# Performance work log

Hardware: AMD Instinct MI355X
Metric: run time of the kernel (lower is better)

## Reference

```python
import jax, jax.numpy as jnp
import numpy as np

B, T, D = 64, 64, 64
E, HA, HB, OUT = 128, 128, 128, 1
SHORT = 2


def _rn(k, shape, scale=0.05):
    return jax.random.normal(k, shape, dtype=jnp.float32) * scale


def setup_inputs() -> dict:
    key = jax.random.key(0)
    ks = jax.random.split(key, 18)
    return {
        "x": jax.random.normal(ks[0], (B, T, D), dtype=jnp.float32),
        "W_emb": _rn(ks[1], (E, D)), "b_emb": _rn(ks[2], (E,)),
        "Wi_a": _rn(ks[3], (3 * HA, E)), "Wh_a": _rn(ks[4], (3 * HA, HA)),
        "bi_a": _rn(ks[5], (3 * HA,)), "bh_a": _rn(ks[6], (3 * HA,)),
        "Wi_b": _rn(ks[7], (3 * HB, E)), "Wh_b": _rn(ks[8], (3 * HB, HB)),
        "bi_b": _rn(ks[9], (3 * HB,)), "bh_b": _rn(ks[10], (3 * HB,)),
        "Wa": _rn(ks[11], (1, HA)), "ba": _rn(ks[12], (1,)),
        "Wb": _rn(ks[13], (E, HB)), "bb": _rn(ks[14], (E,)),
        "Wo": _rn(ks[15], (OUT, E)), "bo": _rn(ks[16], (OUT,)),
        "short": SHORT,
    }


def _gru_cell(x, h, Wi, Wh, bi, bh):
    # PyTorch GRU cell: gates ordered (r, z, n)
    gi = x @ Wi.T + bi
    gh = h @ Wh.T + bh
    ir, iz, in_ = jnp.split(gi, 3, axis=-1)
    hr, hz, hn = jnp.split(gh, 3, axis=-1)
    r = jax.nn.sigmoid(ir + hr)
    z = jax.nn.sigmoid(iz + hz)
    n = jnp.tanh(in_ + r * hn)
    return (1.0 - z) * n + z * h


def _forward(x, W_emb, b_emb, Wi_a, Wh_a, bi_a, bh_a, Wi_b, Wh_b, bi_b, bh_b,
             Wa, ba, Wb, bb, Wo, bo, short):
    Bn, Tn = x.shape[0], x.shape[1]
    temp = jnp.transpose(x, (1, 0, 2))            # [T, B, D]
    emb = temp @ W_emb.T + b_emb                  # [T, B, E]
    P = Tn - 1                                    # prefix p handles att_timesteps t = p+1
    S = Tn - 1                                    # max reversed-prefix length
    p_idx = jnp.arange(P)
    h0a = jnp.zeros((P, Bn, Wh_a.shape[1]), x.dtype)
    h0b = jnp.zeros((P, Bn, Wh_b.shape[1]), x.dtype)

    # All prefixes at once: for prefix p, reversed input at step s is emb[p - s].
    def step(carry, s):
        ha, hb = carry
        j = jnp.clip(p_idx - s, 0, Tn - 1)        # [P]
        e_in = emb[j]                             # [P, B, E]
        x_in = temp[j]                            # [P, B, D]
        na = _gru_cell(e_in, ha, Wi_a, Wh_a, bi_a, bh_a)
        nb = _gru_cell(e_in, hb, Wi_b, Wh_b, bi_b, bh_b)
        valid = (p_idx >= s)[:, None, None]
        ha = jnp.where(valid, na, ha)
        hb = jnp.where(valid, nb, hb)
        return (ha, hb), (ha, hb, e_in, x_in)

    _, (Ha, Hb, Eg, Xg) = jax.lax.scan(step, (h0a, h0b), jnp.arange(S))
    Ha = 0.5 * Ha                                 # reverse_h_a * 0.5, [S, P, B, HA]
    Hb = 0.5 * Hb                                 # reverse_h_b * 0.5, [S, P, B, HB]

    mask = p_idx[None, :] >= jnp.arange(S)[:, None]   # [S, P] valid scan steps
    preA = jnp.einsum('spbh,h->spb', Ha, Wa[0]) + ba[0]
    preA = jnp.where(mask[:, :, None], preA, -jnp.inf)
    alpha = jax.nn.softmax(preA, axis=0)              # softmax over prefix positions
    beta = jnp.tanh(jnp.einsum('spbh,eh->spbe', Hb, Wb) + bb)  # [S, P, B, E]

    # context: c[p] = sum_s alpha * beta * emb[p-s]  (softmax is order-invariant)
    c = jnp.einsum('spb,spbe->pbe', alpha, beta * Eg)          # [P, B, E]
    pred = c @ Wo.T + bo                                        # [P, B, 1]

    # interpretability weights: e = (beta * w_out) @ W_emb, f = alpha*e*x, g = mean over prefix
    e_chain = jnp.einsum('spbe,ed->spbd', beta * Wo[0], W_emb)  # [S, P, B, D]
    f = alpha[..., None] * e_chain * Xg
    g = jnp.sum(f, axis=0) / (p_idx[:, None, None] + 1.0)       # mean over t = p+1 steps

    pred = jnp.transpose(pred[short + 1:], (1, 0, 2))           # [B, T-2-short, 1]
    weight = jnp.transpose(g[short + 1:], (1, 0, 2))            # [B, T-2-short, D]
    return pred, weight


def reference(x, W_emb, b_emb, Wi_a, Wh_a, bi_a, bh_a, Wi_b, Wh_b, bi_b, bh_b,
              Wa, ba, Wb, bb, Wo, bo, short):
    return _forward(x, W_emb, b_emb, Wi_a, Wh_a, bi_a, bh_a, Wi_b, Wh_b, bi_b,
                    bh_b, Wa, ba, Wb, bb, Wo, bo, short)
```

## Files before the change

### kernel.cpp

```cpp
#include <hip/hip_runtime.h>
#include <hip/hip_bf16.h>
#include <math.h>

#define B_ 64
#define T_ 64
#define D_ 64
#define PMIN 3
#define NPOUT 60
#define NCHUNK 8

typedef __hip_bfloat16 bf16;
typedef __attribute__((ext_vector_type(4))) short s16x4;
typedef __attribute__((ext_vector_type(8))) short s16x8;
typedef __attribute__((ext_vector_type(4))) float f32x4;

#define OFF_EMB   0
#define OFF_WIC   524288
#define OFF_XT    622592
#define OFF_GIPK  884736
#define OFF_WPK   2457600
#define OFF_BPPK  2506752
#define OFF_WMPK  2514944
#define OFF_WALPK 2519040
#define OFF_FLAG  2520064

__device__ __forceinline__ float bf2f(unsigned short u) {
    union { float f; unsigned u32; } x; x.u32 = ((unsigned)u) << 16; return x.f;
}
__device__ __forceinline__ unsigned short f2bf(float f) {
    union { float f; unsigned u; } x; x.f = f;
    unsigned r = x.u + 0x7FFFu + ((x.u >> 16) & 1u);
    return (unsigned short)(r >> 16);
}
__device__ __forceinline__ float LDF(const void* p, int i, int flag) {
    return flag ? ((const float*)p)[i] : bf2f(((const unsigned short*)p)[i]);
}
__device__ __forceinline__ float sigmoidf_(float v) { return 1.f / (1.f + __expf(-v)); }
__device__ __forceinline__ float tanhf_(float v) {
    float e = __expf(-2.f * fabsf(v));
    float t = (1.f - e) / (1.f + e);
    return copysignf(t, v);
}
__device__ __forceinline__ int kpi(int s) {
    return (s & ~31) | ((s & 1) << 4) | ((s & 31) >> 1);
}
__device__ __forceinline__ s16x8 ldA(const short* p) {
    s16x4 lo = *(const s16x4*)p;
    s16x4 hi = *(const s16x4*)(p + 4);
    return __builtin_shufflevector(lo, hi, 0, 1, 2, 3, 4, 5, 6, 7);
}

__global__ void detect_dtype(const unsigned short* xr, int* flag)
{
    int tid = threadIdx.x;
    int bad = 0;
    for (int i = tid; i < 4096; i += 256) {
        int ex = (xr[i] >> 7) & 0xFF;
        if (ex >= 140) bad++;
    }
    __shared__ int s[256];
    s[tid] = bad;
    __syncthreads();
    for (int st = 128; st > 0; st >>= 1) {
        if (tid < st) s[tid] += s[tid + st];
        __syncthreads();
    }
    if (tid == 0) *flag = (s[0] > 4) ? 1 : 0;
}

__global__ void prep_all(const void* p_x, const void* p_wemb, const void* p_bemb,
                         const void* p_wia, const void* p_wha,
                         const void* p_wib, const void* p_whb,
                         const void* p_wa, const void* p_wb, const void* p_wo,
                         float* ws, const int* flagp)
{
    const int flag = *flagp;
    int id = blockIdx.x * 256 + threadIdx.x;
    if (id < 98304) {
        int e = id / 768, g = id % 768;
        float v = (g < 384) ? LDF(p_wia, g * 128 + e, flag)
                            : LDF(p_wib, (g - 384) * 128 + e, flag);
        ws[OFF_WIC + id] = v;
    } else if (id < 622592) {
        int id2 = id - 98304;
        int e = id2 & 127;
        int tb = id2 >> 7;
        int b = tb & 63, t = tb >> 6;
        float acc = LDF(p_bemb, e, flag);
        if (flag) {
            const float* xp = (const float*)p_x + (b * T_ + t) * D_;
            const float* wp = (const float*)p_wemb + e * D_;
            #pragma unroll
            for (int d = 0; d < 64; d += 4) {
                f32x4 xv = *(const f32x4*)(xp + d);
                f32x4 wv = *(const f32x4*)(wp + d);
                acc += xv[0]*wv[0] + xv[1]*wv[1] + xv[2]*wv[2] + xv[3]*wv[3];
            }
        } else {
            const unsigned short* xp = (const unsigned short*)p_x + (b * T_ + t) * D_;
            const unsigned short* wp = (const unsigned short*)p_wemb + e * D_;
            for (int d = 0; d < 64; d++) acc += bf2f(xp[d]) * bf2f(wp[d]);
        }
        ws[OFF_EMB + id2] = acc;
    } else if (id < 884736) {
        int id5 = id - 622592;
        int b = id5 & 63, d = (id5 >> 6) & 63, t = id5 >> 12;
        ws[OFF_XT + id5] = LDF(p_x, (b * 64 + t) * 64 + d, flag);
    } else if (id < 983040) {
        unsigned short* wpk = (unsigned short*)(ws + OFF_WPK);
        int id3 = id - 884736;
        int w = id3 / 12288, r1 = id3 % 12288;
        int nt = r1 / 2048, r2 = r1 % 2048;
        int kt = r2 / 512, r3 = r2 % 512;
        int lane = r3 >> 3, j = r3 & 7;
        int cell = w >> 2, wv = w & 3;
        int gate = nt >> 1, tt = nt & 1;
        int g = gate * 128 + wv * 32 + tt * 16 + (lane & 15);
        int k = kpi(kt * 32 + (lane >> 4) * 8 + j);
        wpk[id3] = f2bf(LDF(cell ? p_whb : p_wha, g * 128 + k, flag));
    } else if (id < 999424) {
        unsigned short* bpk = (unsigned short*)(ws + OFF_BPPK);
        int id4 = id - 983040;
        int w = id4 / 2048, r = id4 % 2048;
        int kt = r / 512, lane = (r % 512) >> 3, j = r & 7;
        int e = w * 16 + (lane & 15);
        int k = kpi(kt * 32 + (lane >> 4) * 8 + j);
        bpk[id4] = f2bf(LDF(p_wb, e * 128 + k, flag));
    } else if (id < 1007616) {
        unsigned short* wmk = (unsigned short*)(ws + OFF_WMPK);
        int id6 = id - 999424;
        int nt = id6 / 2048, r = id6 % 2048;
        int kt = r / 512, lane = (r % 512) >> 3, j = r & 7;
        int d = nt * 16 + (lane & 15);
        int e = kt * 32 + (lane >> 4) * 8 + j;
        wmk[id6] = f2bf(LDF(p_wo, e, flag) * LDF(p_wemb, e * 64 + d, flag));
    } else {
        unsigned short* alk = (unsigned short*)(ws + OFF_WALPK);
        int id7 = id - 1007616;
        int kt = id7 / 512, lane = (id7 % 512) >> 3, j = id7 & 7;
        int k = kpi(kt * 32 + (lane >> 4) * 8 + j);
        alk[id7] = ((lane & 15) == 0) ? f2bf(LDF(p_wa, k, flag)) : (unsigned short)0;
    }
}

__global__ void prep_gi(float* ws, const void* p_bia, const void* p_bha,
                        const void* p_bib, const void* p_bhb, const int* flagp)
{
    const int flag = *flagp;
    unsigned short* gipk = (unsigned short*)(ws + OFF_GIPK);
    int t = blockIdx.x >> 3;
    int chunk = blockIdx.x & 7;
    int b0 = chunk * 8;
    int tid = threadIdx.x;
    __shared__ __align__(16) float semT[128][8];
    __shared__ __align__(16) unsigned short stg[6144];
    #pragma unroll
    for (int q = 0; q < 4; q++) {
        int idx = tid + q * 256;
        int r = idx & 7, e = idx >> 3;
        semT[e][r] = ws[OFF_EMB + (size_t)((t * 64 + b0 + r) * 128) + e];
    }
    __syncthreads();
    float acc[3][8];
    #pragma unroll
    for (int g3 = 0; g3 < 3; g3++)
        #pragma unroll
        for (int r = 0; r < 8; r++) acc[g3][r] = 0.f;
    const float* wic = ws + OFF_WIC;
    #pragma unroll 2
    for (int e = 0; e < 128; e++) {
        f32x4 h0 = *(const f32x4*)&semT[e][0];
        f32x4 h1 = *(const f32x4*)&semT[e][4];
        float hv[8] = {h0[0],h0[1],h0[2],h0[3], h1[0],h1[1],h1[2],h1[3]};
        float w0 = wic[e * 768 + tid];
        float w1 = wic[e * 768 + tid + 256];
        float w2 = wic[e * 768 + tid + 512];
        #pragma unroll
        for (int r = 0; r < 8; r++) {
            acc[0][r] += hv[r] * w0;
            acc[1][r] += hv[r] * w1;
            acc[2][r] += hv[r] * w2;
        }
    }
    #pragma unroll
    for (int g3 = 0; g3 < 3; g3++) {
        int g = tid + g3 * 256;
        int cellg = g / 384, gr = g % 384;
        int gate = gr / 128, kh = gr % 128;
        int wvp = kh / 32, tt2 = (kh % 32) / 16, l15p = kh % 16;
        int wq = cellg * 4 + wvp;
        float bias = LDF(cellg ? p_bib : p_bia, gr, flag);
        if (gate < 2) bias += LDF(cellg ? p_bhb : p_bha, gr, flag);
        #pragma unroll
        for (int r = 0; r < 8; r++) {
            float v = acc[g3][r] + bias;
            int lane2 = (r >> 2) * 16 + l15p;
            int slot = gate * 8 + tt2 * 4 + (r & 3);
            stg[(wq * 32 + lane2) * 24 + slot] = f2bf(v);
        }
    }
    __syncthreads();
    const uint4* s4 = (const uint4*)stg;
    uint4* d4 = (uint4*)(gipk + (size_t)(t * 8 + chunk) * 6144);
    for (int i = tid; i < 768; i += 256) d4[i] = s4[i];
}


__launch_bounds__(512, 2)
__global__ void chain_kernel(const float* ws, void* outv, const int* flagp,
                             const void* p_bha, const void* p_bhb,
                             const void* p_bb, const void* p_ba,
                             const void* p_bo, const void* p_wo)
{
    const int p = PMIN + (NPOUT - 1) - (int)blockIdx.x / NCHUNK;
    const int chunk = (int)blockIdx.x % NCHUNK;
    const int tid = threadIdx.x;
    const int lane = tid & 63;
    const int w = tid >> 6;
    const int cell = w >> 2;
    const int wv = w & 3;
    const int l15 = lane & 15;
    const int quad = lane >> 4;

    __shared__ __align__(16) short hbf[2][2][16][132];
    __shared__ __align__(16) short betbf[2][16][132];
    __shared__ __align__(16) short sWm[4][4][64][8];
    __shared__ float spaLds[2][8];

    const unsigned short* gipk = (const unsigned short*)(ws + OFF_GIPK);
    const unsigned short* wpk  = (const unsigned short*)(ws + OFF_WPK);
    const unsigned short* bpk  = (const unsigned short*)(ws + OFF_BPPK);
    const unsigned short* alk  = (const unsigned short*)(ws + OFF_WALPK);
    const int flag = *flagp;

    {
        const int* s2 = (const int*)(ws + OFF_WMPK);
        int* d2 = (int*)&sWm[0][0][0][0];
        for (int i = tid; i < 4096; i += 512) d2[i] = s2[i];
        int* hz = (int*)&hbf[0][0][0][0];
        for (int i = tid; i < 4224; i += 512) hz[i] = 0;
        int* bz = (int*)&betbf[0][0][0];
        for (int i = tid; i < 2112; i += 512) bz[i] = 0;
    }

    s16x8 wB[6][4];
    #pragma unroll
    for (int nt = 0; nt < 6; nt++)
        #pragma unroll
        for (int kt = 0; kt < 4; kt++)
            wB[nt][kt] = *(const s16x8*)(wpk + (((w * 6 + nt) * 4 + kt) * 64 + lane) * 8);
    s16x8 bBp[4], wAl[4];
    #pragma unroll
    for (int kt = 0; kt < 4; kt++) {
        bBp[kt] = *(const s16x8*)(bpk + ((w * 4 + kt) * 64 + lane) * 8);
        wAl[kt] = *(const s16x8*)(alk + (kt * 64 + lane) * 8);
    }

    float bhn0, bhn1, bbE, baf, bof;
    if (flag) {
        const float* bh = (const float*)(cell ? p_bhb : p_bha);
        bhn0 = bh[256 + wv * 32 + l15];
        bhn1 = bh[256 + wv * 32 + 16 + l15];
        bbE = ((const float*)p_bb)[w * 16 + l15];
        baf = ((const float*)p_ba)[0];
        bof = ((const float*)p_bo)[0];
    } else {
        const unsigned short* bh = (const unsigned short*)(cell ? p_bhb : p_bha);
        bhn0 = bf2f(bh[256 + wv * 32 + l15]);
        bhn1 = bf2f(bh[256 + wv * 32 + 16 + l15]);
        bbE = bf2f(((const unsigned short*)p_bb)[w * 16 + l15]);
        baf = bf2f(((const unsigned short*)p_ba)[0]);
        bof = bf2f(((const unsigned short*)p_bo)[0]);
    }

    float h_old[8];
    #pragma unroll
    for (int i = 0; i < 8; i++) h_old[i] = 0.f;
    float accR[9];
    #pragma unroll
    for (int i = 0; i < 9; i++) accR[i] = 0.f;

    __syncthreads();

    for (int it = 0; it <= p + 1; it++) {
        const int j = p - it;
        const int jp = j + 1;
        const bool doGru = (j >= 0);
        const bool doAcc = (it > 0);
        const int cur = it & 1;
        const int nxt = cur ^ 1;
        const int dbuf = it & 1;

        s16x8 giv[3];
        if (doGru) {
            const unsigned short* gp =
                gipk + ((((size_t)j * 8 + chunk) * 8 + w) * 32 + (lane & 31)) * 24;
            #pragma unroll
            for (int i = 0; i < 3; i++) giv[i] = *(const s16x8*)(gp + i * 8);
        }
        f32x4 xv, em0, em1;
        if (doAcc) {
            if (w < 4) {
                xv = *(const f32x4*)(ws + OFF_XT + ((size_t)jp * 64 + w * 16 + l15) * 64
                                     + chunk * 8 + (quad & 1) * 4);
            } else {
                const int row8 = (quad * 4 + (w - 4)) & 7;
                const float* ep = ws + OFF_EMB
                                  + ((size_t)jp * 64 + chunk * 8 + row8) * 128 + l15 * 8;
                em0 = *(const f32x4*)ep;
                em1 = *(const f32x4*)(ep + 4);
            }
        }

        f32x4 Cg[6], Cbp, Cal;
        #pragma unroll
        for (int nt = 0; nt < 6; nt++) Cg[nt] = (f32x4){0.f,0.f,0.f,0.f};
        Cbp = (f32x4){0.f,0.f,0.f,0.f};
        Cal = (f32x4){0.f,0.f,0.f,0.f};

        #pragma unroll
        for (int kt = 0; kt < 4; kt++) {
            s16x8 aB = ldA(&hbf[cur][1][l15][kt * 32 + quad * 8]);
            s16x8 aA;
            if (cell == 0 || w == 7) aA = ldA(&hbf[cur][0][l15][kt * 32 + quad * 8]);
            else aA = aB;
            s16x8 aOwn = cell ? aB : aA;
            #pragma unroll
            for (int nt = 0; nt < 6; nt++)
                Cg[nt] = __builtin_amdgcn_mfma_f32_16x16x32_bf16(aOwn, wB[nt][kt], Cg[nt], 0, 0, 0);
            Cbp = __builtin_amdgcn_mfma_f32_16x16x32_bf16(aB, bBp[kt], Cbp, 0, 0, 0);
            if (w == 7)
                Cal = __builtin_amdgcn_mfma_f32_16x16x32_bf16(aA, wAl[kt], Cal, 0, 0, 0);
        }

        if (w == 7 && l15 == 0 && quad < 2) {
            #pragma unroll
            for (int reg = 0; reg < 4; reg++)
                spaLds[dbuf][quad * 4 + reg] = fminf(0.5f * Cal[reg] + baf, 60.f);
        }
        if (doGru && quad < 2) {
            #pragma unroll
            for (int reg = 0; reg < 4; reg++) {
                float hn2[2];
                #pragma unroll
                for (int tt = 0; tt < 2; tt++) {
                    float gir = bf2f((unsigned short)giv[0][tt * 4 + reg]);
                    float giz = bf2f((unsigned short)giv[1][tt * 4 + reg]);
                    float gin = bf2f((unsigned short)giv[2][tt * 4 + reg]);
                    float ghr = Cg[0 + tt][reg];
                    float ghz = Cg[2 + tt][reg];
                    float ghn = Cg[4 + tt][reg] + (tt ? bhn1 : bhn0);
                    float ho  = h_old[tt * 4 + reg];
                    float rr = sigmoidf_(gir + ghr);
                    float zz = sigmoidf_(giz + ghz);
                    float nn = tanhf_(gin + rr * ghn);
                    float hv2 = (1.f - zz) * nn + zz * ho;
                    h_old[tt * 4 + reg] = hv2;
                    hn2[tt] = hv2;
                }
                unsigned pk = (unsigned)f2bf(hn2[0]) | ((unsigned)f2bf(hn2[1]) << 16);
                *(unsigned*)&hbf[nxt][cell][quad * 4 + reg][wv * 32 + l15 * 2] = pk;
            }
        }
        if (quad < 2) {
            #pragma unroll
            for (int reg = 0; reg < 4; reg++) {
                float bv = tanhf_(0.5f * Cbp[reg] + bbE);
                betbf[dbuf][quad * 4 + reg][w * 16 + l15] = (short)f2bf(bv);
            }
        }

        __syncthreads();

        if (doAcc) {
            if (w < 4) {
                f32x4 ec = (f32x4){0.f,0.f,0.f,0.f};
                #pragma unroll
                for (int kt = 0; kt < 4; kt++) {
                    s16x8 a = ldA(&betbf[dbuf][l15][kt * 32 + quad * 8]);
                    s16x8 bw = *(const s16x8*)&sWm[w][kt][lane][0];
                    ec = __builtin_amdgcn_mfma_f32_16x16x32_bf16(a, bw, ec, 0, 0, 0);
                }
                #pragma unroll
                for (int reg = 0; reg < 4; reg++) {
                    float we = __expf(spaLds[dbuf][(quad * 4 + reg) & 7]);
                    accR[4 + reg] += we;
                    accR[reg] += we * ec[reg] * xv[reg];
                }
            } else {
                const int row8 = (quad * 4 + (w - 4)) & 7;
                float we = __expf(spaLds[dbuf][row8]);
                accR[8] += we;
                const short* bp2 = &betbf[dbuf][row8][l15 * 8];
                s16x4 blo = *(const s16x4*)bp2;
                s16x4 bhi = *(const s16x4*)(bp2 + 4);
                #pragma unroll
                for (int v = 0; v < 4; v++)
                    accR[v] += we * bf2f((unsigned short)blo[v]) * em0[v];
                #pragma unroll
                for (int v = 0; v < 4; v++)
                    accR[4 + v] += we * bf2f((unsigned short)bhi[v]) * em1[v];
            }
        }
    }

    if (w >= 4) {
        const int row = quad * 4 + (w - 4);
        float wo8[8];
        if (flag) {
            const float* wp = (const float*)p_wo + l15 * 8;
            #pragma unroll
            for (int v = 0; v < 8; v++) wo8[v] = wp[v];
        } else {
            const unsigned short* wp = (const unsigned short*)p_wo + l15 * 8;
            #pragma unroll
            for (int v = 0; v < 8; v++) wo8[v] = bf2f(wp[v]);
        }
        float part = 0.f;
        #pragma unroll
        for (int v = 0; v < 8; v++) part += accR[v] * wo8[v];
        part += __shfl_xor(part, 1);
        part += __shfl_xor(part, 2);
        part += __shfl_xor(part, 4);
        part += __shfl_xor(part, 8);
        if (l15 == 0 && row < 8) {
            int bglob = chunk * 8 + row;
            float pr = part / accR[8] + bof;
            size_t oi = (size_t)bglob * NPOUT + (p - PMIN);
            if (flag) ((float*)outv)[oi] = pr;
            else      ((bf16*)outv)[oi] = __float2bfloat16(pr);
        }
    } else if (quad < 2) {
        const float invt = 1.f / (float)(p + 1);
        #pragma unroll
        for (int reg = 0; reg < 4; reg++) {
            int row = quad * 4 + reg;
            int bglob = chunk * 8 + row;
            float gv = accR[reg] / accR[4 + reg] * invt;
            size_t oi = (size_t)B_ * NPOUT
                      + ((size_t)bglob * NPOUT + (p - PMIN)) * 64 + w * 16 + l15;
            if (flag) ((float*)outv)[oi] = gv;
            else      ((bf16*)outv)[oi] = __float2bfloat16(gv);
        }
    }
}

extern "C" void kernel_launch(void* const* d_in, const int* in_sizes, int n_in,
                              void* d_out, int out_size, void* d_ws, size_t ws_size,
                              hipStream_t stream)
{
    float* ws = (float*)d_ws;
    int* flagp = (int*)(ws + OFF_FLAG);

    hipLaunchKernelGGL(detect_dtype, dim3(1), dim3(256), 0, stream,
                       (const unsigned short*)d_in[0], flagp);
    hipLaunchKernelGGL(prep_all, dim3(3944), dim3(256), 0, stream,
                       d_in[0], d_in[1], d_in[2], d_in[3], d_in[4],
                       d_in[7], d_in[8], d_in[11], d_in[13], d_in[15],
                       ws, flagp);
    hipLaunchKernelGGL(prep_gi, dim3(512), dim3(256), 0, stream,
                       ws, d_in[5], d_in[6], d_in[9], d_in[10], flagp);
    hipLaunchKernelGGL(chain_kernel, dim3(NPOUT * NCHUNK), dim3(512), 0, stream,
                       ws, d_out, flagp,
                       d_in[6], d_in[10], d_in[14], d_in[12], d_in[16], d_in[15]);
}
```

Baseline: 354.5 us.

## Fold log2e scaling into weights, split GRU gates across all quads, fuse embedding into prep_gi

Pre-scales the recurrent, beta and attention weights and biases by log2(e) factors so the sigmoid, tanh and softmax use exp2 and a hardware reciprocal directly. The GRU update now runs on all four quads, exchanging the second-tile gate results by lane shuffle instead of having half the lanes each do two tiles. The embedding GEMM moves from prep_all into prep_gi with shared-memory staging, and the input-gate weights are read in their original row-major layout with vectorised loads. LDS row padding changes from 132 to 136 so A-operand reads become single 16-byte loads. Together these aim to cut transcendental cost and idle lanes in the serial recurrence and to shrink the prep kernels, but bf16 rounding of the pre-scaled weights may change accuracy slightly.

```diff
diff --git a/kernel.cpp b/kernel.cpp
--- a/kernel.cpp
+++ b/kernel.cpp
@@ -9,13 +9,16 @@
 #define NPOUT 60
 #define NCHUNK 8
 
+#define LOG2E     1.4426950408889634f
+#define TWOLOG2E  2.8853900817779268f
+
 typedef __hip_bfloat16 bf16;
 typedef __attribute__((ext_vector_type(4))) short s16x4;
 typedef __attribute__((ext_vector_type(8))) short s16x8;
 typedef __attribute__((ext_vector_type(4))) float f32x4;
 
 #define OFF_EMB   0
-#define OFF_WIC   524288
+#define OFF_WIC2  524288
 #define OFF_XT    622592
 #define OFF_GIPK  884736
 #define OFF_WPK   2457600
@@ -35,19 +38,14 @@
 __device__ __forceinline__ float LDF(const void* p, int i, int flag) {
     return flag ? ((const float*)p)[i] : bf2f(((const unsigned short*)p)[i]);
 }
-__device__ __forceinline__ float sigmoidf_(float v) { return 1.f / (1.f + __expf(-v)); }
-__device__ __forceinline__ float tanhf_(float v) {
-    float e = __expf(-2.f * fabsf(v));
-    float t = (1.f - e) / (1.f + e);
-    return copysignf(t, v);
+__device__ __forceinline__ float sig2(float xneg) {
+    return __builtin_amdgcn_rcpf(1.f + __builtin_exp2f(xneg));
+}
+__device__ __forceinline__ float tanh2(float x2) {
+    return 1.f - 2.f * __builtin_amdgcn_rcpf(1.f + __builtin_exp2f(x2));
 }
 __device__ __forceinline__ int kpi(int s) {
     return (s & ~31) | ((s & 1) << 4) | ((s & 31) >> 1);
-}
-__device__ __forceinline__ s16x8 ldA(const short* p) {
-    s16x4 lo = *(const s16x4*)p;
-    s16x4 hi = *(const s16x4*)(p + 4);
-    return __builtin_shufflevector(lo, hi, 0, 1, 2, 3, 4, 5, 6, 7);
 }
 
 __global__ void detect_dtype(const unsigned short* xr, int* flag)
@@ -68,47 +66,25 @@
     if (tid == 0) *flag = (s[0] > 4) ? 1 : 0;
 }
 
-__global__ void prep_all(const void* p_x, const void* p_wemb, const void* p_bemb,
-                         const void* p_wia, const void* p_wha,
-                         const void* p_wib, const void* p_whb,
+__global__ void prep_all(const void* p_x, const void* p_wemb,
+                         const void* p_wia, const void* p_wib,
+                         const void* p_wha, const void* p_whb,
                          const void* p_wa, const void* p_wb, const void* p_wo,
                          float* ws, const int* flagp)
 {
     const int flag = *flagp;
     int id = blockIdx.x * 256 + threadIdx.x;
     if (id < 98304) {
-        int e = id / 768, g = id % 768;
-        float v = (g < 384) ? LDF(p_wia, g * 128 + e, flag)
-                            : LDF(p_wib, (g - 384) * 128 + e, flag);
-        ws[OFF_WIC + id] = v;
-    } else if (id < 622592) {
-        int id2 = id - 98304;
-        int e = id2 & 127;
-        int tb = id2 >> 7;
-        int b = tb & 63, t = tb >> 6;
-        float acc = LDF(p_bemb, e, flag);
-        if (flag) {
-            const float* xp = (const float*)p_x + (b * T_ + t) * D_;
-            const float* wp = (const float*)p_wemb + e * D_;
-            #pragma unroll
-            for (int d = 0; d < 64; d += 4) {
-                f32x4 xv = *(const f32x4*)(xp + d);
-                f32x4 wv = *(const f32x4*)(wp + d);
-                acc += xv[0]*wv[0] + xv[1]*wv[1] + xv[2]*wv[2] + xv[3]*wv[3];
-            }
-        } else {
-            const unsigned short* xp = (const unsigned short*)p_x + (b * T_ + t) * D_;
-            const unsigned short* wp = (const unsigned short*)p_wemb + e * D_;
-            for (int d = 0; d < 64; d++) acc += bf2f(xp[d]) * bf2f(wp[d]);
-        }
-        ws[OFF_EMB + id2] = acc;
-    } else if (id < 884736) {
-        int id5 = id - 622592;
+        float v = (id < 49152) ? LDF(p_wia, id, flag)
+                               : LDF(p_wib, id - 49152, flag);
+        ws[OFF_WIC2 + id] = v;
+    } else if (id < 360448) {
+        int id5 = id - 98304;
         int b = id5 & 63, d = (id5 >> 6) & 63, t = id5 >> 12;
         ws[OFF_XT + id5] = LDF(p_x, (b * 64 + t) * 64 + d, flag);
-    } else if (id < 983040) {
+    } else if (id < 458752) {
         unsigned short* wpk = (unsigned short*)(ws + OFF_WPK);
-        int id3 = id - 884736;
+        int id3 = id - 360448;
         int w = id3 / 12288, r1 = id3 % 12288;
         int nt = r1 / 2048, r2 = r1 % 2048;
         int kt = r2 / 512, r3 = r2 % 512;
@@ -117,18 +93,19 @@
         int gate = nt >> 1, tt = nt & 1;
         int g = gate * 128 + wv * 32 + tt * 16 + (lane & 15);
         int k = kpi(kt * 32 + (lane >> 4) * 8 + j);
-        wpk[id3] = f2bf(LDF(cell ? p_whb : p_wha, g * 128 + k, flag));
-    } else if (id < 999424) {
+        float sc = (gate < 2) ? -LOG2E : TWOLOG2E;
+        wpk[id3] = f2bf(sc * LDF(cell ? p_whb : p_wha, g * 128 + k, flag));
+    } else if (id < 475136) {
         unsigned short* bpk = (unsigned short*)(ws + OFF_BPPK);
-        int id4 = id - 983040;
+        int id4 = id - 458752;
         int w = id4 / 2048, r = id4 % 2048;
         int kt = r / 512, lane = (r % 512) >> 3, j = r & 7;
         int e = w * 16 + (lane & 15);
         int k = kpi(kt * 32 + (lane >> 4) * 8 + j);
-        bpk[id4] = f2bf(LDF(p_wb, e * 128 + k, flag));
-    } else if (id < 1007616) {
+        bpk[id4] = f2bf(LOG2E * LDF(p_wb, e * 128 + k, flag));
+    } else if (id < 483328) {
         unsigned short* wmk = (unsigned short*)(ws + OFF_WMPK);
-        int id6 = id - 999424;
+        int id6 = id - 475136;
         int nt = id6 / 2048, r = id6 % 2048;
         int kt = r / 512, lane = (r % 512) >> 3, j = r & 7;
         int d = nt * 16 + (lane & 15);
@@ -136,14 +113,16 @@
         wmk[id6] = f2bf(LDF(p_wo, e, flag) * LDF(p_wemb, e * 64 + d, flag));
     } else {
         unsigned short* alk = (unsigned short*)(ws + OFF_WALPK);
-        int id7 = id - 1007616;
+        int id7 = id - 483328;
         int kt = id7 / 512, lane = (id7 % 512) >> 3, j = id7 & 7;
         int k = kpi(kt * 32 + (lane >> 4) * 8 + j);
-        alk[id7] = ((lane & 15) == 0) ? f2bf(LDF(p_wa, k, flag)) : (unsigned short)0;
-    }
-}
-
-__global__ void prep_gi(float* ws, const void* p_bia, const void* p_bha,
+        alk[id7] = ((lane & 15) == 0) ? f2bf(0.5f * LOG2E * LDF(p_wa, k, flag))
+                                      : (unsigned short)0;
+    }
+}
+
+__global__ void prep_gi(float* ws, const void* p_x, const void* p_wemb,
+                        const void* p_bemb, const void* p_bia, const void* p_bha,
                         const void* p_bib, const void* p_bhb, const int* flagp)
 {
     const int flag = *flagp;
@@ -152,35 +131,57 @@
     int chunk = blockIdx.x & 7;
     int b0 = chunk * 8;
     int tid = threadIdx.x;
-    __shared__ __align__(16) float semT[128][8];
+    __shared__ __align__(16) float sX[8][64];
+    __shared__ __align__(16) float sWe[128][64];
+    __shared__ __align__(16) float semT2[8][132];
     __shared__ __align__(16) unsigned short stg[6144];
+
+    for (int i = tid; i < 512; i += 256) {
+        int r = i >> 6, d = i & 63;
+        sX[r][d] = LDF(p_x, ((b0 + r) * 64 + t) * 64 + d, flag);
+    }
+    for (int i = tid; i < 8192; i += 256)
+        sWe[i >> 6][i & 63] = LDF(p_wemb, i, flag);
+    __syncthreads();
+
     #pragma unroll
     for (int q = 0; q < 4; q++) {
-        int idx = tid + q * 256;
-        int r = idx & 7, e = idx >> 3;
-        semT[e][r] = ws[OFF_EMB + (size_t)((t * 64 + b0 + r) * 128) + e];
+        int o = tid + q * 256;
+        int e = o & 127, r = o >> 7;
+        float acc = LDF(p_bemb, e, flag);
+        #pragma unroll
+        for (int d = 0; d < 64; d += 4) {
+            f32x4 xv = *(const f32x4*)&sX[r][d];
+            f32x4 wv = *(const f32x4*)&sWe[e][d];
+            acc += xv[0]*wv[0] + xv[1]*wv[1] + xv[2]*wv[2] + xv[3]*wv[3];
+        }
+        semT2[r][e] = acc;
+        ws[OFF_EMB + (size_t)((t * 64 + b0 + r) * 128) + e] = acc;
     }
     __syncthreads();
-    float acc[3][8];
+
+    float acc3[3][8];
     #pragma unroll
     for (int g3 = 0; g3 < 3; g3++)
         #pragma unroll
-        for (int r = 0; r < 8; r++) acc[g3][r] = 0.f;
-    const float* wic = ws + OFF_WIC;
+        for (int r = 0; r < 8; r++) acc3[g3][r] = 0.f;
+    const float* w2 = ws + OFF_WIC2;
     #pragma unroll 2
-    for (int e = 0; e < 128; e++) {
-        f32x4 h0 = *(const f32x4*)&semT[e][0];
-        f32x4 h1 = *(const f32x4*)&semT[e][4];
-        float hv[8] = {h0[0],h0[1],h0[2],h0[3], h1[0],h1[1],h1[2],h1[3]};
-        float w0 = wic[e * 768 + tid];
-        float w1 = wic[e * 768 + tid + 256];
-        float w2 = wic[e * 768 + tid + 512];
-        #pragma unroll
-        for (int r = 0; r < 8; r++) {
-            acc[0][r] += hv[r] * w0;
-            acc[1][r] += hv[r] * w1;
-            acc[2][r] += hv[r] * w2;
-        }
+    for (int e0 = 0; e0 < 128; e0 += 4) {
+        f32x4 wv0 = *(const f32x4*)(w2 + (size_t)(tid      ) * 128 + e0);
+        f32x4 wv1 = *(const f32x4*)(w2 + (size_t)(tid + 256) * 128 + e0);
+        f32x4 wv2 = *(const f32x4*)(w2 + (size_t)(tid + 512) * 128 + e0);
+        f32x4 h[8];
+        #pragma unroll
+        for (int r = 0; r < 8; r++) h[r] = *(const f32x4*)&semT2[r][e0];
+        #pragma unroll
+        for (int r = 0; r < 8; r++)
+            #pragma unroll
+            for (int c = 0; c < 4; c++) {
+                acc3[0][r] += wv0[c] * h[r][c];
+                acc3[1][r] += wv1[c] * h[r][c];
+                acc3[2][r] += wv2[c] * h[r][c];
+            }
     }
     #pragma unroll
     for (int g3 = 0; g3 < 3; g3++) {
@@ -191,9 +192,10 @@
         int wq = cellg * 4 + wvp;
         float bias = LDF(cellg ? p_bib : p_bia, gr, flag);
         if (gate < 2) bias += LDF(cellg ? p_bhb : p_bha, gr, flag);
+        float sc = (gate < 2) ? -LOG2E : TWOLOG2E;
         #pragma unroll
         for (int r = 0; r < 8; r++) {
-            float v = acc[g3][r] + bias;
+            float v = sc * (acc3[g3][r] + bias);
             int lane2 = (r >> 2) * 16 + l15p;
             int slot = gate * 8 + tt2 * 4 + (r & 3);
             stg[(wq * 32 + lane2) * 24 + slot] = f2bf(v);
@@ -221,9 +223,11 @@
     const int wv = w & 3;
     const int l15 = lane & 15;
     const int quad = lane >> 4;
-
-    __shared__ __align__(16) short hbf[2][2][16][132];
-    __shared__ __align__(16) short betbf[2][16][132];
+    const int tt = quad >> 1;
+    const int rquad = quad & 1;
+
+    __shared__ __align__(16) short hbf[2][2][16][136];
+    __shared__ __align__(16) short betbf[2][16][136];
     __shared__ __align__(16) short sWm[4][4][64][8];
     __shared__ float spaLds[2][8];
 
@@ -238,9 +242,9 @@
         int* d2 = (int*)&sWm[0][0][0][0];
         for (int i = tid; i < 4096; i += 512) d2[i] = s2[i];
         int* hz = (int*)&hbf[0][0][0][0];
-        for (int i = tid; i < 4224; i += 512) hz[i] = 0;
+        for (int i = tid; i < 4352; i += 512) hz[i] = 0;
         int* bz = (int*)&betbf[0][0][0];
-        for (int i = tid; i < 2112; i += 512) bz[i] = 0;
+        for (int i = tid; i < 2176; i += 512) bz[i] = 0;
     }
 
     s16x8 wB[6][4];
@@ -256,26 +260,15 @@
         wAl[kt] = *(const s16x8*)(alk + (kt * 64 + lane) * 8);
     }
 
-    float bhn0, bhn1, bbE, baf, bof;
-    if (flag) {
-        const float* bh = (const float*)(cell ? p_bhb : p_bha);
-        bhn0 = bh[256 + wv * 32 + l15];
-        bhn1 = bh[256 + wv * 32 + 16 + l15];
-        bbE = ((const float*)p_bb)[w * 16 + l15];
-        baf = ((const float*)p_ba)[0];
-        bof = ((const float*)p_bo)[0];
-    } else {
-        const unsigned short* bh = (const unsigned short*)(cell ? p_bhb : p_bha);
-        bhn0 = bf2f(bh[256 + wv * 32 + l15]);
-        bhn1 = bf2f(bh[256 + wv * 32 + 16 + l15]);
-        bbE = bf2f(((const unsigned short*)p_bb)[w * 16 + l15]);
-        baf = bf2f(((const unsigned short*)p_ba)[0]);
-        bof = bf2f(((const unsigned short*)p_bo)[0]);
-    }
-
-    float h_old[8];
-    #pragma unroll
-    for (int i = 0; i < 8; i++) h_old[i] = 0.f;
+    const float bhnS = TWOLOG2E *
+        LDF(cell ? p_bhb : p_bha, 256 + wv * 32 + tt * 16 + l15, flag);
+    const float bbE2 = TWOLOG2E * LDF(p_bb, w * 16 + l15, flag);
+    const float bafS = LOG2E * LDF(p_ba, 0, flag);
+    const float bof  = LDF(p_bo, 0, flag);
+
+    float h_old[4];
+    #pragma unroll
+    for (int i = 0; i < 4; i++) h_old[i] = 0.f;
     float accR[9];
     #pragma unroll
     for (int i = 0; i < 9; i++) accR[i] = 0.f;
@@ -291,18 +284,19 @@
         const int nxt = cur ^ 1;
         const int dbuf = it & 1;
 
-        s16x8 giv[3];
+        s16x4 giv[3];
         if (doGru) {
-            const unsigned short* gp =
+            const unsigned short* gp0 =
                 gipk + ((((size_t)j * 8 + chunk) * 8 + w) * 32 + (lane & 31)) * 24;
-            #pragma unroll
-            for (int i = 0; i < 3; i++) giv[i] = *(const s16x8*)(gp + i * 8);
+            giv[0] = *(const s16x4*)(gp0 + tt * 4);
+            giv[1] = *(const s16x4*)(gp0 + 8 + tt * 4);
+            giv[2] = *(const s16x4*)(gp0 + 16 + tt * 4);
         }
         f32x4 xv, em0, em1;
         if (doAcc) {
             if (w < 4) {
                 xv = *(const f32x4*)(ws + OFF_XT + ((size_t)jp * 64 + w * 16 + l15) * 64
-                                     + chunk * 8 + (quad & 1) * 4);
+                                     + chunk * 8 + rquad * 4);
             } else {
                 const int row8 = (quad * 4 + (w - 4)) & 7;
                 const float* ep = ws + OFF_EMB
@@ -320,9 +314,9 @@
 
         #pragma unroll
         for (int kt = 0; kt < 4; kt++) {
-            s16x8 aB = ldA(&hbf[cur][1][l15][kt * 32 + quad * 8]);
+            s16x8 aB = *(const s16x8*)&hbf[cur][1][l15][kt * 32 + quad * 8];
             s16x8 aA;
-            if (cell == 0 || w == 7) aA = ldA(&hbf[cur][0][l15][kt * 32 + quad * 8]);
+            if (cell == 0 || w == 7) aA = *(const s16x8*)&hbf[cur][0][l15][kt * 32 + quad * 8];
             else aA = aB;
             s16x8 aOwn = cell ? aB : aA;
             #pragma unroll
@@ -336,36 +330,32 @@
         if (w == 7 && l15 == 0 && quad < 2) {
             #pragma unroll
             for (int reg = 0; reg < 4; reg++)
-                spaLds[dbuf][quad * 4 + reg] = fminf(0.5f * Cal[reg] + baf, 60.f);
-        }
-        if (doGru && quad < 2) {
+                spaLds[dbuf][quad * 4 + reg] = fminf(Cal[reg] + bafS, 86.f);
+        }
+        if (doGru) {
             #pragma unroll
             for (int reg = 0; reg < 4; reg++) {
-                float hn2[2];
-                #pragma unroll
-                for (int tt = 0; tt < 2; tt++) {
-                    float gir = bf2f((unsigned short)giv[0][tt * 4 + reg]);
-                    float giz = bf2f((unsigned short)giv[1][tt * 4 + reg]);
-                    float gin = bf2f((unsigned short)giv[2][tt * 4 + reg]);
-                    float ghr = Cg[0 + tt][reg];
-                    float ghz = Cg[2 + tt][reg];
-                    float ghn = Cg[4 + tt][reg] + (tt ? bhn1 : bhn0);
-                    float ho  = h_old[tt * 4 + reg];
-                    float rr = sigmoidf_(gir + ghr);
-                    float zz = sigmoidf_(giz + ghz);
-                    float nn = tanhf_(gin + rr * ghn);
-                    float hv2 = (1.f - zz) * nn + zz * ho;
-                    h_old[tt * 4 + reg] = hv2;
-                    hn2[tt] = hv2;
-                }
-                unsigned pk = (unsigned)f2bf(hn2[0]) | ((unsigned)f2bf(hn2[1]) << 16);
-                *(unsigned*)&hbf[nxt][cell][quad * 4 + reg][wv * 32 + l15 * 2] = pk;
+                float s1 = __shfl_xor(Cg[1][reg], 32);
+                float s3 = __shfl_xor(Cg[3][reg], 32);
+                float s5 = __shfl_xor(Cg[5][reg], 32);
+                float ghr = tt ? s1 : Cg[0][reg];
+                float ghz = tt ? s3 : Cg[2][reg];
+                float ghn = (tt ? s5 : Cg[4][reg]) + bhnS;
+                float gir = bf2f((unsigned short)giv[0][reg]);
+                float giz = bf2f((unsigned short)giv[1][reg]);
+                float gin = bf2f((unsigned short)giv[2][reg]);
+                float rr = sig2(gir + ghr);
+                float zz = sig2(giz + ghz);
+                float nn = tanh2(gin + rr * ghn);
+                float hv2 = (1.f - zz) * nn + zz * h_old[reg];
+                h_old[reg] = hv2;
+                hbf[nxt][cell][rquad * 4 + reg][wv * 32 + l15 * 2 + tt] = (short)f2bf(hv2);
             }
         }
         if (quad < 2) {
             #pragma unroll
             for (int reg = 0; reg < 4; reg++) {
-                float bv = tanhf_(0.5f * Cbp[reg] + bbE);
+                float bv = tanh2(Cbp[reg] + bbE2);
                 betbf[dbuf][quad * 4 + reg][w * 16 + l15] = (short)f2bf(bv);
             }
         }
@@ -377,19 +367,19 @@
                 f32x4 ec = (f32x4){0.f,0.f,0.f,0.f};
                 #pragma unroll
                 for (int kt = 0; kt < 4; kt++) {
-                    s16x8 a = ldA(&betbf[dbuf][l15][kt * 32 + quad * 8]);
+                    s16x8 a = *(const s16x8*)&betbf[dbuf][l15][kt * 32 + quad * 8];
                     s16x8 bw = *(const s16x8*)&sWm[w][kt][lane][0];
                     ec = __builtin_amdgcn_mfma_f32_16x16x32_bf16(a, bw, ec, 0, 0, 0);
                 }
                 #pragma unroll
                 for (int reg = 0; reg < 4; reg++) {
-                    float we = __expf(spaLds[dbuf][(quad * 4 + reg) & 7]);
+                    float we = __builtin_exp2f(spaLds[dbuf][(quad * 4 + reg) & 7]);
                     accR[4 + reg] += we;
                     accR[reg] += we * ec[reg] * xv[reg];
                 }
             } else {
                 const int row8 = (quad * 4 + (w - 4)) & 7;
-                float we = __expf(spaLds[dbuf][row8]);
+                float we = __builtin_exp2f(spaLds[dbuf][row8]);
                 accR[8] += we;
                 const short* bp2 = &betbf[dbuf][row8][l15 * 8];
                 s16x4 blo = *(const s16x4*)bp2;
@@ -454,12 +444,12 @@
 
     hipLaunchKernelGGL(detect_dtype, dim3(1), dim3(256), 0, stream,
                        (const unsigned short*)d_in[0], flagp);
-    hipLaunchKernelGGL(prep_all, dim3(3944), dim3(256), 0, stream,
-                       d_in[0], d_in[1], d_in[2], d_in[3], d_in[4],
-                       d_in[7], d_in[8], d_in[11], d_in[13], d_in[15],
-                       ws, flagp);
+    hipLaunchKernelGGL(prep_all, dim3(1896), dim3(256), 0, stream,
+                       d_in[0], d_in[1], d_in[3], d_in[7], d_in[4], d_in[8],
+                       d_in[11], d_in[13], d_in[15], ws, flagp);
     hipLaunchKernelGGL(prep_gi, dim3(512), dim3(256), 0, stream,
-                       ws, d_in[5], d_in[6], d_in[9], d_in[10], flagp);
+                       ws, d_in[0], d_in[1], d_in[2], d_in[5], d_in[6],
+                       d_in[9], d_in[10], flagp);
     hipLaunchKernelGGL(chain_kernel, dim3(NPOUT * NCHUNK), dim3(512), 0, stream,
                        ws, d_out, flagp,
                        d_in[6], d_in[10], d_in[14], d_in[12], d_in[16], d_in[15]);
```

New measurement: 308.4 us. -13.0%, faster.
